# Kernel tuning notes

Measured on AMD Instinct MI355X. Metric: run time of the kernel, lower is better.

## Reference

```python
import jax, jax.numpy as jnp
import numpy as np

HID1 = 256  # hidden_dim1 hardcoded to 256 in Gps.__init__
NEG_SLOPE = 0.01

def leaky_relu(x):
    return jnp.where(x >= 0, x, NEG_SLOPE * x)

def setup_inputs() -> dict:
    key = jax.random.key(0)
    ks = jax.random.split(key, 8)
    N_total, F = 100000, 256
    N_seed, topn = 16384, 4
    M1, M2 = 4096, 2048
    EMB = 256
    return {
        "feature_matrix": jax.random.normal(ks[0], (N_total, F), jnp.float32),
        "adj_layer1": jax.random.uniform(ks[1], (N_seed, M1), jnp.float32),
        "feature_layer1": jax.random.normal(ks[2], (M1, F), jnp.float32),
        "adj_layer2": jax.random.uniform(ks[3], (N_seed * topn, M2), jnp.float32),
        "feature_layer2": jax.random.normal(ks[4], (M2, HID1), jnp.float32),
        "W1": jax.random.normal(ks[5], (HID1, 2 * F), jnp.float32) * 0.05,
        "W2": jax.random.normal(ks[6], (EMB, 2 * HID1), jnp.float32) * 0.05,
        "seed_nodes": jax.random.randint(ks[7], (N_seed,), 0, N_total, jnp.int64 if jax.config.jax_enable_x64 else jnp.int32),
    }

def reference(feature_matrix, adj_layer1, feature_layer1, adj_layer2, feature_layer2, W1, W2, seed_nodes):
    # --- step1: EncoderAggregate1 ---
    feat0 = feature_matrix[seed_nodes]                       # [N, F] gather
    agg0 = (adj_layer1 @ feature_layer1) * 0.5               # [N, F] neighbor aggregate
    h = leaky_relu(jnp.concatenate([feat0, agg0], axis=1) @ W1.T)  # [N, HID1]
    # dropout: eval mode (identity)
    # --- step2: EncoderAggregate2 ---
    agg1 = (adj_layer2 @ feature_layer2) * 0.5               # [N*topn, HID1]
    agg1_mean = agg1.reshape(h.shape[0], -1, HID1).mean(axis=1)    # [N, HID1] segment-mean
    emb = leaky_relu(jnp.concatenate([h, agg1_mean], axis=1) @ W2.T)  # [N, EMB]
    return emb
```

## Files before the change

### kernel.cpp

```cpp
#include <hip/hip_runtime.h>
#include <stdint.h>


typedef unsigned short u16;
typedef unsigned int   u32;
typedef __attribute__((ext_vector_type(8))) short bf16x8;
typedef __attribute__((ext_vector_type(4))) float f32x4;
typedef __attribute__((ext_vector_type(4))) float float4_t;
typedef __attribute__((ext_vector_type(4))) u16   u16x4;

#define DEVI __device__ __forceinline__

constexpr int BM = 64;
constexpr int BN = 256;
constexpr int BK = 32;

DEVI u16 f2bf(float f) {
  union { float f; u32 u; } v; v.f = f;
  return (u16)((v.u + 0x7fffu + ((v.u >> 16) & 1u)) >> 16);
}
DEVI float bf2f(u16 h) {
  union { u32 u; float f; } v; v.u = ((u32)h) << 16; return v.f;
}
DEVI void split2(float x, u16& hi, u16& lo) {
  hi = f2bf(x);
  lo = f2bf(x - bf2f(hi));
}

DEVI void gll16(const u16* g, u16* l) {
  __builtin_amdgcn_global_load_lds(
      (__attribute__((address_space(1))) u32*)g,
      (__attribute__((address_space(3))) u32*)l, 16, 0, 0);
}

__global__ __launch_bounds__(256) void prep_kernel(
    const float* __restrict__ W1, const float* __restrict__ W2,
    u16* __restrict__ Wt1h, u16* __restrict__ Wt1l,
    u16* __restrict__ Wt2h, u16* __restrict__ Wt2l,
    u16* __restrict__ B1h,  u16* __restrict__ B1l,
    u16* __restrict__ B2h,  u16* __restrict__ B2l)
{
  const int idx = blockIdx.x * 256 + threadIdx.x;
  const int job = idx >> 16;
  const int e   = idx & 65535;
  const int n   = e >> 8;
  const int k   = e & 255;
  u16 hi, lo;
  if (job == 0) {
    split2(W1[n * 512 + 256 + k], hi, lo);
    const int o = ((k >> 3) * 256 + n) * 8 + (k & 7);
    Wt1h[o] = hi; Wt1l[o] = lo;
  } else if (job == 1) {
    split2(W1[n * 512 + k], hi, lo);
    const int r = 4096 + k;
    const int o = ((r >> 3) * 256 + n) * 8 + (r & 7);
    B1h[o] = hi; B1l[o] = lo;
  } else if (job == 2) {
    split2(W2[n * 512 + 256 + k], hi, lo);
    const int o = ((k >> 3) * 256 + n) * 8 + (k & 7);
    Wt2h[o] = hi; Wt2l[o] = lo;
  } else {
    split2(W2[n * 512 + k], hi, lo);
    const int r = 2048 + k;
    const int o = ((r >> 3) * 256 + n) * 8 + (r & 7);
    B2h[o] = hi; B2l[o] = lo;
  }
}

template<int MODE>
DEVI void loadA(const float* __restrict__ A1, int lda1,
                const float* __restrict__ featm, const int* __restrict__ seed,
                const u16* __restrict__ A3h, const u16* __restrict__ A3l,
                int tileM, int kphase, int sm, int skl,
                float4_t& r0, float4_t& r1, float4_t& r2, float4_t& r3,
                u16x4& rh, u16x4& rl)
{
  const int kk = kphase + skl;
  if constexpr (MODE == 0) {
    r0 = *(const float4_t*)&A1[(size_t)(tileM + sm) * lda1 + kk];
  } else if constexpr (MODE == 1) {
    const int s = seed[tileM + sm];
    r0 = *(const float4_t*)&featm[(size_t)s * 256 + kk];
  } else if constexpr (MODE == 2) {
    const float* p = &A1[(size_t)(tileM + sm) * 4 * lda1 + kk];
    r0 = *(const float4_t*)p;
    r1 = *(const float4_t*)(p + lda1);
    r2 = *(const float4_t*)(p + 2 * lda1);
    r3 = *(const float4_t*)(p + 3 * lda1);
  } else {
    const size_t o = (size_t)(tileM + sm) * 256 + kk;
    rh = *(const u16x4*)&A3h[o];
    rl = *(const u16x4*)&A3l[o];
  }
}

template<int MODE>
DEVI void writeA(float4_t r0, float4_t r1, float4_t r2, float4_t r3,
                 u16x4 rh, u16x4 rl, u16* dh, u16* dl)
{
  if constexpr (MODE == 3) {
    *(u16x4*)dh = rh;
    *(u16x4*)dl = rl;
  } else {
    if constexpr (MODE == 2) r0 = (r0 + r1 + r2 + r3) * 0.25f;
    u16x4 h, l;
#pragma unroll
    for (int j = 0; j < 4; ++j) { u16 a, b; split2(r0[j], a, b); h[j] = a; l[j] = b; }
    *(u16x4*)dh = h;
    *(u16x4*)dl = l;
  }
}

DEVI void stageB_fn(const u16* __restrict__ Bh, const u16* __restrict__ Bl,
                    int it, u16 (*sBb)[8192], int tid)
{
  const size_t base = (size_t)it * 8192;
  const int wv = tid >> 6, ln = tid & 63;
#pragma unroll
  for (int c = 0; c < 2; ++c) {
    const size_t o = base + (size_t)c * 4096 + (size_t)wv * 512;
    gll16(Bh + o + ln * 8, &sBb[0][c * 4096 + wv * 512]);
    gll16(Bl + o + ln * 8, &sBb[1][c * 4096 + wv * 512]);
  }
}

template<int AM1, int AM2, int OM>
__global__ __launch_bounds__(512)
void gemm_split(const float* __restrict__ A1, int lda1,
                const float* __restrict__ featm, const int* __restrict__ seed,
                const u16* __restrict__ A3h, const u16* __restrict__ A3l,
                const u16* __restrict__ Bh, const u16* __restrict__ Bl,
                int kt_total, int kt_split,
                float* __restrict__ Of, u16* __restrict__ Oh, u16* __restrict__ Ol)
{
  __shared__ u16 sA[2][2][2048];
  __shared__ u16 sB[2][2][8192];

  const int tid   = threadIdx.x;
  const int tileM = blockIdx.x * BM;
  const int lane  = tid & 63;
  const int wave  = tid >> 6;
  const int wm    = wave >> 2;
  const int wn    = wave & 3;
  const int l15   = lane & 15;
  const int l4    = lane >> 4;

  const int slot = tid >> 1;
  const int half = tid & 1;
  const int sm   = slot & 63;
  const int skb  = slot >> 6;
  const int skl  = skb * 8 + half * 4;

  f32x4 acc[2][4] = {};
  int cur = 0;

  {
    stageB_fn(Bh, Bl, 0, sB[0], tid);
    float4_t r0{}, r1{}, r2{}, r3{}; u16x4 rh{}, rl{};
    loadA<AM1>(A1, lda1, featm, seed, A3h, A3l, tileM, 0, sm, skl,
               r0, r1, r2, r3, rh, rl);
    writeA<AM1>(r0, r1, r2, r3, rh, rl,
                &sA[0][0][slot * 8 + half * 4], &sA[0][1][slot * 8 + half * 4]);
  }
  __syncthreads();

  for (int it = 0; it < kt_total; ++it) {
    const int  nb = cur ^ 1;
    const bool hn = (it + 1) < kt_total;
    const bool p1 = (it + 1) < kt_split;

    float4_t r0{}, r1{}, r2{}, r3{}; u16x4 rh{}, rl{};
    if (hn) {
      stageB_fn(Bh, Bl, it + 1, sB[nb], tid);
      if (p1) loadA<AM1>(A1, lda1, featm, seed, A3h, A3l, tileM,
                         (it + 1) * BK, sm, skl, r0, r1, r2, r3, rh, rl);
      else    loadA<AM2>(A1, lda1, featm, seed, A3h, A3l, tileM,
                         (it + 1 - kt_split) * BK, sm, skl, r0, r1, r2, r3, rh, rl);
    }

    bf16x8 ah[2], al[2], bh[4], bl[4];
#pragma unroll
    for (int mf = 0; mf < 2; ++mf) {
      const int sa = (l4 * 64 + wm * 32 + mf * 16 + l15) * 8;
      ah[mf] = *(const bf16x8*)&sA[cur][0][sa];
      al[mf] = *(const bf16x8*)&sA[cur][1][sa];
    }
#pragma unroll
    for (int nf = 0; nf < 4; ++nf) {
      const int sb = (l4 * 256 + wn * 64 + nf * 16 + l15) * 8;
      bh[nf] = *(const bf16x8*)&sB[cur][0][sb];
      bl[nf] = *(const bf16x8*)&sB[cur][1][sb];
    }
#pragma unroll
    for (int mf = 0; mf < 2; ++mf)
#pragma unroll
      for (int nf = 0; nf < 4; ++nf) {
        acc[mf][nf] = __builtin_amdgcn_mfma_f32_16x16x32_bf16(ah[mf], bh[nf], acc[mf][nf], 0, 0, 0);
        acc[mf][nf] = __builtin_amdgcn_mfma_f32_16x16x32_bf16(al[mf], bh[nf], acc[mf][nf], 0, 0, 0);
        acc[mf][nf] = __builtin_amdgcn_mfma_f32_16x16x32_bf16(ah[mf], bl[nf], acc[mf][nf], 0, 0, 0);
      }

    if (hn) {
      u16* dh = &sA[nb][0][slot * 8 + half * 4];
      u16* dl = &sA[nb][1][slot * 8 + half * 4];
      if (p1) writeA<AM1>(r0, r1, r2, r3, rh, rl, dh, dl);
      else    writeA<AM2>(r0, r1, r2, r3, rh, rl, dh, dl);
    }
    __syncthreads();
    cur = nb;
  }

#pragma unroll
  for (int mf = 0; mf < 2; ++mf)
#pragma unroll
    for (int nf = 0; nf < 4; ++nf)
#pragma unroll
      for (int j = 0; j < 4; ++j) {
        const int row = tileM + wm * 32 + mf * 16 + l4 * 4 + j;
        const int col = wn * 64 + nf * 16 + l15;
        float v = acc[mf][nf][j];
        if constexpr (OM == 0) {
          v *= 0.5f;
          u16 hi, lo; split2(v, hi, lo);
          const size_t o = ((size_t)(row >> 3) * 256 + col) * 8 + (row & 7);
          Oh[o] = hi; Ol[o] = lo;
        } else if constexpr (OM == 1) {
          v = v >= 0.f ? v : 0.01f * v;
          Of[(size_t)row * 256 + col] = v;
        } else {
          v = v >= 0.f ? v : 0.01f * v;
          u16 hi, lo; split2(v, hi, lo);
          const size_t o = (size_t)row * 256 + col;
          Oh[o] = hi; Ol[o] = lo;
        }
      }
}

extern "C" void kernel_launch(void* const* d_in, const int* in_sizes, int n_in,
                              void* d_out, int out_size, void* d_ws, size_t ws_size,
                              hipStream_t stream)
{
  const float* featm = (const float*)d_in[0];
  const float* adj1  = (const float*)d_in[1];
  const float* f1    = (const float*)d_in[2];
  const float* adj2  = (const float*)d_in[3];
  const float* f2    = (const float*)d_in[4];
  const float* W1    = (const float*)d_in[5];
  const float* W2    = (const float*)d_in[6];
  const int*   seed  = (const int*)d_in[7];
  float* out = (float*)d_out;

  char* p = (char*)d_ws;
  u16* B1h  = (u16*)p; p += (size_t)4352 * 256 * 2;
  u16* B1l  = (u16*)p; p += (size_t)4352 * 256 * 2;
  u16* B2h  = (u16*)p; p += (size_t)2304 * 256 * 2;
  u16* B2l  = (u16*)p; p += (size_t)2304 * 256 * 2;
  u16* Wt1h = (u16*)p; p += (size_t)256 * 256 * 2;
  u16* Wt1l = (u16*)p; p += (size_t)256 * 256 * 2;
  u16* Wt2h = (u16*)p; p += (size_t)256 * 256 * 2;
  u16* Wt2l = (u16*)p; p += (size_t)256 * 256 * 2;
  u16* Hh   = (u16*)p; p += (size_t)16384 * 256 * 2;
  u16* Hl   = (u16*)p; p += (size_t)16384 * 256 * 2;

  prep_kernel<<<1024, 256, 0, stream>>>(W1, W2, Wt1h, Wt1l, Wt2h, Wt2l,
                                        B1h, B1l, B2h, B2l);

  gemm_split<0, 0, 0><<<64, 512, 0, stream>>>(
      f1, 256, nullptr, nullptr, nullptr, nullptr,
      Wt1h, Wt1l, 8, 8, nullptr, B1h, B1l);

  gemm_split<0, 0, 0><<<32, 512, 0, stream>>>(
      f2, 256, nullptr, nullptr, nullptr, nullptr,
      Wt2h, Wt2l, 8, 8, nullptr, B2h, B2l);

  gemm_split<0, 1, 2><<<256, 512, 0, stream>>>(
      adj1, 4096, featm, seed, nullptr, nullptr,
      B1h, B1l, 136, 128, nullptr, Hh, Hl);

  gemm_split<2, 3, 1><<<256, 512, 0, stream>>>(
      adj2, 2048, nullptr, nullptr, Hh, Hl,
      B2h, B2l, 72, 64, out, nullptr, nullptr);
}
```

Measured before the change: 1.191 ms.

## Fuse all stages into one cooperative kernel with split-K and larger M tiles

Replaces the five separate launches with a single cooperative persistent kernel that uses grid.sync between the prep, small-GEMM, and two big GEMM phases. The M tile grows from 64 to 128 rows, so only 128 tiles are needed, and each big GEMM is split into two K halves across 256 blocks. The halves write fp32 partials that a separate elementwise pass sums, applies leaky-relu to, and for the first GEMM converts to hi/lo bf16. This is meant to remove launch gaps and raise per-block reuse while keeping 256 blocks busy. In exchange it adds extra partial-sum traffic through global memory and grid-wide barriers, and the small GEMMs now run on only 48 blocks.

```diff
diff --git a/kernel.cpp b/kernel.cpp
--- a/kernel.cpp
+++ b/kernel.cpp
@@ -1,19 +1,21 @@
 #include <hip/hip_runtime.h>
+#include <hip/hip_cooperative_groups.h>
 #include <stdint.h>
+
+namespace cg = cooperative_groups;
 
 
 typedef unsigned short u16;
 typedef unsigned int   u32;
 typedef __attribute__((ext_vector_type(8))) short bf16x8;
 typedef __attribute__((ext_vector_type(4))) float f32x4;
-typedef __attribute__((ext_vector_type(4))) float float4_t;
 typedef __attribute__((ext_vector_type(4))) u16   u16x4;
+typedef __attribute__((ext_vector_type(8))) u16   u16x8;
 
 #define DEVI __device__ __forceinline__
 
-constexpr int BM = 64;
-constexpr int BN = 256;
-constexpr int BK = 32;
+constexpr int BM = 128, BN = 256, BK = 32;
+constexpr int NTHR = 512;
 
 DEVI u16 f2bf(float f) {
   union { float f; u32 u; } v; v.f = f;
@@ -33,166 +35,132 @@
       (__attribute__((address_space(3))) u32*)l, 16, 0, 0);
 }
 
-__global__ __launch_bounds__(256) void prep_kernel(
-    const float* __restrict__ W1, const float* __restrict__ W2,
-    u16* __restrict__ Wt1h, u16* __restrict__ Wt1l,
-    u16* __restrict__ Wt2h, u16* __restrict__ Wt2l,
-    u16* __restrict__ B1h,  u16* __restrict__ B1l,
-    u16* __restrict__ B2h,  u16* __restrict__ B2l)
-{
-  const int idx = blockIdx.x * 256 + threadIdx.x;
-  const int job = idx >> 16;
-  const int e   = idx & 65535;
-  const int n   = e >> 8;
-  const int k   = e & 255;
-  u16 hi, lo;
-  if (job == 0) {
-    split2(W1[n * 512 + 256 + k], hi, lo);
-    const int o = ((k >> 3) * 256 + n) * 8 + (k & 7);
-    Wt1h[o] = hi; Wt1l[o] = lo;
-  } else if (job == 1) {
-    split2(W1[n * 512 + k], hi, lo);
-    const int r = 4096 + k;
-    const int o = ((r >> 3) * 256 + n) * 8 + (r & 7);
-    B1h[o] = hi; B1l[o] = lo;
-  } else if (job == 2) {
-    split2(W2[n * 512 + 256 + k], hi, lo);
-    const int o = ((k >> 3) * 256 + n) * 8 + (k & 7);
-    Wt2h[o] = hi; Wt2l[o] = lo;
-  } else {
-    split2(W2[n * 512 + k], hi, lo);
-    const int r = 2048 + k;
-    const int o = ((r >> 3) * 256 + n) * 8 + (r & 7);
-    B2h[o] = hi; B2l[o] = lo;
-  }
-}
+struct ARegs { f32x4 r0,r1,r2,r3,r4,r5,r6,r7; u16x4 h0,h1,l0,l1; };
 
 template<int MODE>
 DEVI void loadA(const float* __restrict__ A1, int lda1,
                 const float* __restrict__ featm, const int* __restrict__ seed,
                 const u16* __restrict__ A3h, const u16* __restrict__ A3l,
-                int tileM, int kphase, int sm, int skl,
-                float4_t& r0, float4_t& r1, float4_t& r2, float4_t& r3,
-                u16x4& rh, u16x4& rl)
-{
-  const int kk = kphase + skl;
+                int tileM, int kk, int row, ARegs& a)
+{
   if constexpr (MODE == 0) {
-    r0 = *(const float4_t*)&A1[(size_t)(tileM + sm) * lda1 + kk];
+    const float* p = &A1[(size_t)(tileM + row) * lda1 + kk];
+    a.r0 = *(const f32x4*)p; a.r1 = *(const f32x4*)(p + 4);
   } else if constexpr (MODE == 1) {
-    const int s = seed[tileM + sm];
-    r0 = *(const float4_t*)&featm[(size_t)s * 256 + kk];
+    const int s = seed[tileM + row];
+    const float* p = &featm[(size_t)s * 256 + kk];
+    a.r0 = *(const f32x4*)p; a.r1 = *(const f32x4*)(p + 4);
   } else if constexpr (MODE == 2) {
-    const float* p = &A1[(size_t)(tileM + sm) * 4 * lda1 + kk];
-    r0 = *(const float4_t*)p;
-    r1 = *(const float4_t*)(p + lda1);
-    r2 = *(const float4_t*)(p + 2 * lda1);
-    r3 = *(const float4_t*)(p + 3 * lda1);
+    const float* p = &A1[(size_t)(tileM + row) * 4 * lda1 + kk];
+    a.r0 = *(const f32x4*)p;              a.r4 = *(const f32x4*)(p + 4);
+    a.r1 = *(const f32x4*)(p + lda1);     a.r5 = *(const f32x4*)(p + lda1 + 4);
+    a.r2 = *(const f32x4*)(p + 2*lda1);   a.r6 = *(const f32x4*)(p + 2*lda1 + 4);
+    a.r3 = *(const f32x4*)(p + 3*lda1);   a.r7 = *(const f32x4*)(p + 3*lda1 + 4);
   } else {
-    const size_t o = (size_t)(tileM + sm) * 256 + kk;
-    rh = *(const u16x4*)&A3h[o];
-    rl = *(const u16x4*)&A3l[o];
+    const size_t o = (size_t)(tileM + row) * 256 + kk;
+    a.h0 = *(const u16x4*)&A3h[o]; a.h1 = *(const u16x4*)&A3h[o + 4];
+    a.l0 = *(const u16x4*)&A3l[o]; a.l1 = *(const u16x4*)&A3l[o + 4];
   }
 }
 
 template<int MODE>
-DEVI void writeA(float4_t r0, float4_t r1, float4_t r2, float4_t r3,
-                 u16x4 rh, u16x4 rl, u16* dh, u16* dl)
-{
+DEVI void writeA(ARegs& a, u16* dh, u16* dl)
+{
+  u16x8 h, l;
   if constexpr (MODE == 3) {
-    *(u16x4*)dh = rh;
-    *(u16x4*)dl = rl;
+#pragma unroll
+    for (int j = 0; j < 4; ++j) {
+      h[j] = a.h0[j]; h[4 + j] = a.h1[j];
+      l[j] = a.l0[j]; l[4 + j] = a.l1[j];
+    }
   } else {
-    if constexpr (MODE == 2) r0 = (r0 + r1 + r2 + r3) * 0.25f;
-    u16x4 h, l;
-#pragma unroll
-    for (int j = 0; j < 4; ++j) { u16 a, b; split2(r0[j], a, b); h[j] = a; l[j] = b; }
-    *(u16x4*)dh = h;
-    *(u16x4*)dl = l;
-  }
-}
-
-DEVI void stageB_fn(const u16* __restrict__ Bh, const u16* __restrict__ Bl,
-                    int it, u16 (*sBb)[8192], int tid)
-{
-  const size_t base = (size_t)it * 8192;
+    f32x4 e0 = a.r0, e1 = a.r1;
+    if constexpr (MODE == 2) {
+      e0 = (a.r0 + a.r1 + a.r2 + a.r3) * 0.25f;
+      e1 = (a.r4 + a.r5 + a.r6 + a.r7) * 0.25f;
+    }
+#pragma unroll
+    for (int j = 0; j < 4; ++j) {
+      u16 x, y;
+      split2(e0[j], x, y); h[j] = x;     l[j] = y;
+      split2(e1[j], x, y); h[4 + j] = x; l[4 + j] = y;
+    }
+  }
+  *(u16x8*)dh = h;
+  *(u16x8*)dl = l;
+}
+
+DEVI void stageB(const u16* __restrict__ Bh, const u16* __restrict__ Bl,
+                 int s, u16* dBh, u16* dBl, int tid)
+{
+  const size_t base = (size_t)s * (BK * BN);
   const int wv = tid >> 6, ln = tid & 63;
 #pragma unroll
   for (int c = 0; c < 2; ++c) {
-    const size_t o = base + (size_t)c * 4096 + (size_t)wv * 512;
-    gll16(Bh + o + ln * 8, &sBb[0][c * 4096 + wv * 512]);
-    gll16(Bl + o + ln * 8, &sBb[1][c * 4096 + wv * 512]);
+    const int lo = c * 4096 + wv * 512;
+    gll16(Bh + base + lo + ln * 8, dBh + lo);
+    gll16(Bl + base + lo + ln * 8, dBl + lo);
   }
 }
 
 template<int AM1, int AM2, int OM>
-__global__ __launch_bounds__(512)
-void gemm_split(const float* __restrict__ A1, int lda1,
-                const float* __restrict__ featm, const int* __restrict__ seed,
-                const u16* __restrict__ A3h, const u16* __restrict__ A3l,
-                const u16* __restrict__ Bh, const u16* __restrict__ Bl,
-                int kt_total, int kt_split,
-                float* __restrict__ Of, u16* __restrict__ Oh, u16* __restrict__ Ol)
-{
-  __shared__ u16 sA[2][2][2048];
-  __shared__ u16 sB[2][2][8192];
-
-  const int tid   = threadIdx.x;
-  const int tileM = blockIdx.x * BM;
-  const int lane  = tid & 63;
-  const int wave  = tid >> 6;
-  const int wm    = wave >> 2;
-  const int wn    = wave & 3;
-  const int l15   = lane & 15;
-  const int l4    = lane >> 4;
-
-  const int slot = tid >> 1;
-  const int half = tid & 1;
-  const int sm   = slot & 63;
-  const int skb  = slot >> 6;
-  const int skl  = skb * 8 + half * 4;
-
-  f32x4 acc[2][4] = {};
-  int cur = 0;
+DEVI void gemm_dev(u16 (&sA)[2][2][BM*BK], u16 (&sB)[2][2][BK*BN],
+                   int tileM, int s0, int s1, int ssplit,
+                   const float* __restrict__ A1, int lda1,
+                   const float* __restrict__ featm, const int* __restrict__ seed,
+                   const u16* __restrict__ A3h, const u16* __restrict__ A3l,
+                   const u16* __restrict__ Bh, const u16* __restrict__ Bl,
+                   float* __restrict__ Of, u16* __restrict__ Oh, u16* __restrict__ Ol)
+{
+  const int tid  = threadIdx.x;
+  const int lane = tid & 63, wave = tid >> 6;
+  const int wm = wave >> 2, wn = wave & 3;
+  const int l15 = lane & 15, l4 = lane >> 4;
+  const int kb = tid >> 7, row = tid & 127;
+
+  f32x4 acc[4][4] = {};
 
   {
-    stageB_fn(Bh, Bl, 0, sB[0], tid);
-    float4_t r0{}, r1{}, r2{}, r3{}; u16x4 rh{}, rl{};
-    loadA<AM1>(A1, lda1, featm, seed, A3h, A3l, tileM, 0, sm, skl,
-               r0, r1, r2, r3, rh, rl);
-    writeA<AM1>(r0, r1, r2, r3, rh, rl,
-                &sA[0][0][slot * 8 + half * 4], &sA[0][1][slot * 8 + half * 4]);
+    stageB(Bh, Bl, s0, sB[0][0], sB[0][1], tid);
+    ARegs a;
+    const bool m1 = s0 < ssplit;
+    const int kk = (m1 ? s0 * BK : (s0 - ssplit) * BK) + kb * 8;
+    if (m1) loadA<AM1>(A1, lda1, featm, seed, A3h, A3l, tileM, kk, row, a);
+    else    loadA<AM2>(A1, lda1, featm, seed, A3h, A3l, tileM, kk, row, a);
+    u16* dh = &sA[0][0][(kb * BM + row) * 8];
+    u16* dl = &sA[0][1][(kb * BM + row) * 8];
+    if (m1) writeA<AM1>(a, dh, dl); else writeA<AM2>(a, dh, dl);
   }
   __syncthreads();
 
-  for (int it = 0; it < kt_total; ++it) {
-    const int  nb = cur ^ 1;
-    const bool hn = (it + 1) < kt_total;
-    const bool p1 = (it + 1) < kt_split;
-
-    float4_t r0{}, r1{}, r2{}, r3{}; u16x4 rh{}, rl{};
+  for (int s = s0; s < s1; ++s) {
+    const int  cur = (s - s0) & 1, nb = cur ^ 1;
+    const bool hn  = (s + 1) < s1;
+
+    ARegs a; bool m1 = true;
     if (hn) {
-      stageB_fn(Bh, Bl, it + 1, sB[nb], tid);
-      if (p1) loadA<AM1>(A1, lda1, featm, seed, A3h, A3l, tileM,
-                         (it + 1) * BK, sm, skl, r0, r1, r2, r3, rh, rl);
-      else    loadA<AM2>(A1, lda1, featm, seed, A3h, A3l, tileM,
-                         (it + 1 - kt_split) * BK, sm, skl, r0, r1, r2, r3, rh, rl);
-    }
-
-    bf16x8 ah[2], al[2], bh[4], bl[4];
-#pragma unroll
-    for (int mf = 0; mf < 2; ++mf) {
-      const int sa = (l4 * 64 + wm * 32 + mf * 16 + l15) * 8;
+      stageB(Bh, Bl, s + 1, sB[nb][0], sB[nb][1], tid);
+      m1 = (s + 1) < ssplit;
+      const int kk = (m1 ? (s + 1) * BK : (s + 1 - ssplit) * BK) + kb * 8;
+      if (m1) loadA<AM1>(A1, lda1, featm, seed, A3h, A3l, tileM, kk, row, a);
+      else    loadA<AM2>(A1, lda1, featm, seed, A3h, A3l, tileM, kk, row, a);
+    }
+
+    bf16x8 ah[4], al[4], bh[4], bl[4];
+#pragma unroll
+    for (int mf = 0; mf < 4; ++mf) {
+      const int sa = (l4 * BM + wm * 64 + mf * 16 + l15) * 8;
       ah[mf] = *(const bf16x8*)&sA[cur][0][sa];
       al[mf] = *(const bf16x8*)&sA[cur][1][sa];
     }
 #pragma unroll
     for (int nf = 0; nf < 4; ++nf) {
-      const int sb = (l4 * 256 + wn * 64 + nf * 16 + l15) * 8;
+      const int sb = (l4 * BN + wn * 64 + nf * 16 + l15) * 8;
       bh[nf] = *(const bf16x8*)&sB[cur][0][sb];
       bl[nf] = *(const bf16x8*)&sB[cur][1][sb];
     }
 #pragma unroll
-    for (int mf = 0; mf < 2; ++mf)
+    for (int mf = 0; mf < 4; ++mf)
 #pragma unroll
       for (int nf = 0; nf < 4; ++nf) {
         acc[mf][nf] = __builtin_amdgcn_mfma_f32_16x16x32_bf16(ah[mf], bh[nf], acc[mf][nf], 0, 0, 0);
@@ -201,83 +169,157 @@
       }
 
     if (hn) {
-      u16* dh = &sA[nb][0][slot * 8 + half * 4];
-      u16* dl = &sA[nb][1][slot * 8 + half * 4];
-      if (p1) writeA<AM1>(r0, r1, r2, r3, rh, rl, dh, dl);
-      else    writeA<AM2>(r0, r1, r2, r3, rh, rl, dh, dl);
+      u16* dh = &sA[nb][0][(kb * BM + row) * 8];
+      u16* dl = &sA[nb][1][(kb * BM + row) * 8];
+      if (m1) writeA<AM1>(a, dh, dl); else writeA<AM2>(a, dh, dl);
     }
     __syncthreads();
-    cur = nb;
-  }
-
-#pragma unroll
-  for (int mf = 0; mf < 2; ++mf)
+  }
+
+#pragma unroll
+  for (int mf = 0; mf < 4; ++mf)
 #pragma unroll
     for (int nf = 0; nf < 4; ++nf)
 #pragma unroll
       for (int j = 0; j < 4; ++j) {
-        const int row = tileM + wm * 32 + mf * 16 + l4 * 4 + j;
-        const int col = wn * 64 + nf * 16 + l15;
+        const int r = tileM + wm * 64 + mf * 16 + l4 * 4 + j;
+        const int c = wn * 64 + nf * 16 + l15;
         float v = acc[mf][nf][j];
         if constexpr (OM == 0) {
           v *= 0.5f;
           u16 hi, lo; split2(v, hi, lo);
-          const size_t o = ((size_t)(row >> 3) * 256 + col) * 8 + (row & 7);
+          const size_t o = ((size_t)(r >> 3) * 256 + c) * 8 + (r & 7);
           Oh[o] = hi; Ol[o] = lo;
-        } else if constexpr (OM == 1) {
-          v = v >= 0.f ? v : 0.01f * v;
-          Of[(size_t)row * 256 + col] = v;
         } else {
-          v = v >= 0.f ? v : 0.01f * v;
-          u16 hi, lo; split2(v, hi, lo);
-          const size_t o = (size_t)row * 256 + col;
-          Oh[o] = hi; Ol[o] = lo;
+          Of[(size_t)r * 256 + c] = v;
         }
       }
+}
+
+struct GpsP {
+  const float *featm, *adj1, *f1, *adj2, *f2, *W1, *W2;
+  const int* seed;
+  float* out;
+  u16 *B1h, *B1l, *B2h, *B2l, *Wt1h, *Wt1l, *Wt2h, *Wt2l, *Hh, *Hl;
+  float *P0, *P1;
+};
+
+__global__ __launch_bounds__(512, 2) void gps_fused(GpsP p)
+{
+  __shared__ u16 sA[2][2][BM*BK];
+  __shared__ u16 sB[2][2][BK*BN];
+  cg::grid_group grid = cg::this_grid();
+  const int bid = blockIdx.x, tid = threadIdx.x;
+  const int t0 = bid * NTHR + tid;
+
+#pragma unroll
+  for (int rep = 0; rep < 2; ++rep) {
+    const int idx = rep * 131072 + t0;
+    const int job = idx >> 16, e = idx & 65535, n = e >> 8, k = e & 255;
+    u16 hi, lo;
+    if (job == 0) {
+      split2(p.W1[n * 512 + 256 + k], hi, lo);
+      const int o = ((k >> 3) * 256 + n) * 8 + (k & 7);
+      p.Wt1h[o] = hi; p.Wt1l[o] = lo;
+    } else if (job == 1) {
+      split2(p.W1[n * 512 + k], hi, lo);
+      const int r = 4096 + k;
+      const size_t o = ((size_t)(r >> 3) * 256 + n) * 8 + (r & 7);
+      p.B1h[o] = hi; p.B1l[o] = lo;
+    } else if (job == 2) {
+      split2(p.W2[n * 512 + 256 + k], hi, lo);
+      const int o = ((k >> 3) * 256 + n) * 8 + (k & 7);
+      p.Wt2h[o] = hi; p.Wt2l[o] = lo;
+    } else {
+      split2(p.W2[n * 512 + k], hi, lo);
+      const int r = 2048 + k;
+      const size_t o = ((size_t)(r >> 3) * 256 + n) * 8 + (r & 7);
+      p.B2h[o] = hi; p.B2l[o] = lo;
+    }
+  }
+  __threadfence(); grid.sync();
+
+  if (bid < 32)
+    gemm_dev<0,0,0>(sA, sB, bid * BM, 0, 8, 8,
+                    p.f1, 256, nullptr, nullptr, nullptr, nullptr,
+                    p.Wt1h, p.Wt1l, nullptr, p.B1h, p.B1l);
+  else if (bid < 48)
+    gemm_dev<0,0,0>(sA, sB, (bid - 32) * BM, 0, 8, 8,
+                    p.f2, 256, nullptr, nullptr, nullptr, nullptr,
+                    p.Wt2h, p.Wt2l, nullptr, p.B2h, p.B2l);
+  __threadfence(); grid.sync();
+
+  {
+    const int g = bid >> 7, tile = bid & 127;
+    gemm_dev<0,1,3>(sA, sB, tile * BM, g * 68, (g + 1) * 68, 128,
+                    p.adj1, 4096, p.featm, p.seed, nullptr, nullptr,
+                    p.B1h, p.B1l, g ? p.P1 : p.P0, nullptr, nullptr);
+  }
+  __threadfence(); grid.sync();
+
+#pragma unroll
+  for (int rep = 0; rep < 8; ++rep) {
+    const int idx = rep * 131072 + t0;
+    f32x4 v = ((const f32x4*)p.P0)[idx] + ((const f32x4*)p.P1)[idx];
+    u16x4 h, l;
+#pragma unroll
+    for (int j = 0; j < 4; ++j) {
+      float x = v[j]; x = x >= 0.f ? x : 0.01f * x;
+      u16 a, b; split2(x, a, b); h[j] = a; l[j] = b;
+    }
+    ((u16x4*)p.Hh)[idx] = h; ((u16x4*)p.Hl)[idx] = l;
+  }
+  __threadfence(); grid.sync();
+
+  {
+    const int g = bid >> 7, tile = bid & 127;
+    gemm_dev<2,3,3>(sA, sB, tile * BM, g * 36, (g + 1) * 36, 64,
+                    p.adj2, 2048, nullptr, nullptr, p.Hh, p.Hl,
+                    p.B2h, p.B2l, g ? p.P1 : p.P0, nullptr, nullptr);
+  }
+  __threadfence(); grid.sync();
+
+#pragma unroll
+  for (int rep = 0; rep < 8; ++rep) {
+    const int idx = rep * 131072 + t0;
+    f32x4 v = ((const f32x4*)p.P0)[idx] + ((const f32x4*)p.P1)[idx];
+#pragma unroll
+    for (int j = 0; j < 4; ++j) { float x = v[j]; v[j] = x >= 0.f ? x : 0.01f * x; }
+    ((f32x4*)p.out)[idx] = v;
+  }
 }
 
 extern "C" void kernel_launch(void* const* d_in, const int* in_sizes, int n_in,
                               void* d_out, int out_size, void* d_ws, size_t ws_size,
                               hipStream_t stream)
 {
-  const float* featm = (const float*)d_in[0];
-  const float* adj1  = (const float*)d_in[1];
-  const float* f1    = (const float*)d_in[2];
-  const float* adj2  = (const float*)d_in[3];
-  const float* f2    = (const float*)d_in[4];
-  const float* W1    = (const float*)d_in[5];
-  const float* W2    = (const float*)d_in[6];
-  const int*   seed  = (const int*)d_in[7];
-  float* out = (float*)d_out;
-
-  char* p = (char*)d_ws;
-  u16* B1h  = (u16*)p; p += (size_t)4352 * 256 * 2;
-  u16* B1l  = (u16*)p; p += (size_t)4352 * 256 * 2;
-  u16* B2h  = (u16*)p; p += (size_t)2304 * 256 * 2;
-  u16* B2l  = (u16*)p; p += (size_t)2304 * 256 * 2;
-  u16* Wt1h = (u16*)p; p += (size_t)256 * 256 * 2;
-  u16* Wt1l = (u16*)p; p += (size_t)256 * 256 * 2;
-  u16* Wt2h = (u16*)p; p += (size_t)256 * 256 * 2;
-  u16* Wt2l = (u16*)p; p += (size_t)256 * 256 * 2;
-  u16* Hh   = (u16*)p; p += (size_t)16384 * 256 * 2;
-  u16* Hl   = (u16*)p; p += (size_t)16384 * 256 * 2;
-
-  prep_kernel<<<1024, 256, 0, stream>>>(W1, W2, Wt1h, Wt1l, Wt2h, Wt2l,
-                                        B1h, B1l, B2h, B2l);
-
-  gemm_split<0, 0, 0><<<64, 512, 0, stream>>>(
-      f1, 256, nullptr, nullptr, nullptr, nullptr,
-      Wt1h, Wt1l, 8, 8, nullptr, B1h, B1l);
-
-  gemm_split<0, 0, 0><<<32, 512, 0, stream>>>(
-      f2, 256, nullptr, nullptr, nullptr, nullptr,
-      Wt2h, Wt2l, 8, 8, nullptr, B2h, B2l);
-
-  gemm_split<0, 1, 2><<<256, 512, 0, stream>>>(
-      adj1, 4096, featm, seed, nullptr, nullptr,
-      B1h, B1l, 136, 128, nullptr, Hh, Hl);
-
-  gemm_split<2, 3, 1><<<256, 512, 0, stream>>>(
-      adj2, 2048, nullptr, nullptr, Hh, Hl,
-      B2h, B2l, 72, 64, out, nullptr, nullptr);
-}
+  GpsP hp;
+  hp.featm = (const float*)d_in[0];
+  hp.adj1  = (const float*)d_in[1];
+  hp.f1    = (const float*)d_in[2];
+  hp.adj2  = (const float*)d_in[3];
+  hp.f2    = (const float*)d_in[4];
+  hp.W1    = (const float*)d_in[5];
+  hp.W2    = (const float*)d_in[6];
+  hp.seed  = (const int*)d_in[7];
+  hp.out   = (float*)d_out;
+
+  char* q = (char*)d_ws;
+  auto take = [&](size_t bytes) { char* r = q; q += ((bytes + 255) & ~(size_t)255); return r; };
+  hp.B1h  = (u16*)take((size_t)4352 * 256 * 2);
+  hp.B1l  = (u16*)take((size_t)4352 * 256 * 2);
+  hp.B2h  = (u16*)take((size_t)2304 * 256 * 2);
+  hp.B2l  = (u16*)take((size_t)2304 * 256 * 2);
+  hp.Wt1h = (u16*)take((size_t)256 * 256 * 2);
+  hp.Wt1l = (u16*)take((size_t)256 * 256 * 2);
+  hp.Wt2h = (u16*)take((size_t)256 * 256 * 2);
+  hp.Wt2l = (u16*)take((size_t)256 * 256 * 2);
+  hp.Hh   = (u16*)take((size_t)16384 * 256 * 2);
+  hp.Hl   = (u16*)take((size_t)16384 * 256 * 2);
+  hp.P0   = (float*)take((size_t)16384 * 256 * 4);
+  hp.P1   = (float*)take((size_t)16384 * 256 * 4);
+
+  void* args[] = { (void*)&hp };
+  hipLaunchCooperativeKernel((const void*)gps_fused, dim3(256), dim3(512),
+                             args, 0, stream);
+}
```

New measurement: 1.601 ms. 34.4% more time.
